# Kernel tuning notes

Measured on AMD Instinct MI355X. Metric: run time of the kernel, lower is better.

Reference implementation:

```python
import jax, jax.numpy as jnp
import numpy as np

N_NODES = 8      # objects per graph (fixed in source)
N_AT = 16        # anchors/targets vocab: 8 colors + 8 markers
H = 128          # n_hidden
BS = 16384


def _mlp(x, W1, b1, W2, b2):
    # layers.fully_connected default activation is relu; second layer linear.
    # dropout is identity in eval mode.
    return jax.nn.relu(x @ W1 + b1) @ W2 + b2


def _edges_and_segments(bs):
    # static edge list: all ordered pairs (i,j), i != j, per graph, offset per batch
    ii, jj = np.meshgrid(np.arange(N_NODES), np.arange(N_NODES), indexing='ij')
    m = ii != jj
    base = np.stack([ii[m], jj[m]], axis=1)                      # [56, 2]
    offs = (np.arange(bs) * N_NODES)[:, None, None]
    edges = (base[None] + offs).reshape(-1, 2).astype(np.int32)  # [bs*56, 2]
    seg_ids = np.repeat(np.arange(bs), N_NODES).astype(np.int32) # [bs*8]
    return jnp.asarray(edges), jnp.asarray(seg_ids)


def setup_inputs() -> dict:
    key = jax.random.key(0)
    ks = jax.random.split(key, 14)

    anchors = jax.random.randint(ks[0], (BS,), 0, N_AT)
    n_jumps = jax.random.randint(ks[1], (BS,), 0, N_NODES)
    positions = jax.random.uniform(ks[2], (BS, N_NODES, 2), dtype=jnp.float32)
    colors = jax.random.randint(ks[3], (BS, N_NODES), 0, 8)
    markers = jax.random.randint(ks[4], (BS, N_NODES), 8, 16)  # markers live in [8,16)

    def lin(k, fan_in, fan_out):
        return jax.random.normal(k, (fan_in, fan_out), dtype=jnp.float32) / np.sqrt(fan_in)

    d_in = 2 + 8 + 8 + N_AT + N_NODES  # pos + color_oh + marker_oh + question(16+8) = 42
    z = lambda n: jnp.zeros((n,), jnp.float32)
    return {
        'anchors': anchors, 'n_jumps': n_jumps, 'positions': positions,
        'colors': colors, 'markers': markers,
        'pre_W1': lin(ks[5], d_in, H),     'pre_b1': z(H),
        'pre_W2': lin(ks[6], H, H),        'pre_b2': z(H),
        'msg_W1': lin(ks[7], 2 * H + 1, H),'msg_b1': z(H),
        'msg_W2': lin(ks[8], H, H),        'msg_b2': z(H),
        'post_W1': lin(ks[9], 2 * H, H),   'post_b1': z(H),
        'post_W2': lin(ks[10], H, H),      'post_b2': z(H),
        'out_W1': lin(ks[11], H, H),       'out_b1': z(H),
        'out_W2': lin(ks[12], H, N_AT),    'out_b2': z(N_AT),
    }


def reference(anchors, n_jumps, positions, colors, markers,
              pre_W1, pre_b1, pre_W2, pre_b2,
              msg_W1, msg_b1, msg_W2, msg_b2,
              post_W1, post_b1, post_W2, post_b2,
              out_W1, out_b1, out_W2, out_b2):
    bs = positions.shape[0]
    edges, seg_ids = _edges_and_segments(bs)
    n_total = bs * N_NODES

    col_oh = jax.nn.one_hot(colors, 8, dtype=jnp.float32).reshape(n_total, 8)
    mrk_oh = jax.nn.one_hot(markers - 8, 8, dtype=jnp.float32).reshape(n_total, 8)
    pos = positions.reshape(n_total, 2)

    # pairwise euclidean distance per edge -> [E, 1]
    dp = pos[edges[:, 0]] - pos[edges[:, 1]]
    dist = jnp.sqrt(jnp.sum(dp * dp, axis=1, keepdims=True))

    # question broadcast to every node of its graph
    q = jnp.concatenate([jax.nn.one_hot(anchors, N_AT, dtype=jnp.float32),
                         jax.nn.one_hot(n_jumps, N_NODES, dtype=jnp.float32)], axis=1)
    q = q[seg_ids]  # [bs*8, 24]

    x0 = _mlp(jnp.concatenate([pos, col_oh, mrk_oh, q], axis=1),
              pre_W1, pre_b1, pre_W2, pre_b2)  # [bs*8, H]

    # one message-passing step: gather -> MLP -> scatter(segment_sum on source idx)
    mi = jnp.concatenate([x0[edges[:, 0]], x0[edges[:, 1]], dist], axis=1)  # [E, 257]
    msgs = _mlp(mi, msg_W1, msg_b1, msg_W2, msg_b2)                          # [E, H]
    upd = jax.ops.segment_sum(msgs, edges[:, 0], num_segments=n_total)       # [bs*8, H]

    x = _mlp(jnp.concatenate([upd, x0], axis=1), post_W1, post_b1, post_W2, post_b2)

    logits = jax.ops.segment_sum(x, seg_ids, num_segments=bs)  # [bs, H]
    logits = _mlp(logits, out_W1, out_b1, out_W2, out_b2)      # [bs, 16]
    return logits
```

## Files before the change

### kernel.cpp

```cpp
#include <hip/hip_runtime.h>

#define LROW 136
#define FSTR 72

typedef __bf16 bf16x8  __attribute__((ext_vector_type(8)));
typedef __bf16 bf16x2v __attribute__((ext_vector_type(2)));
typedef float  f32x4   __attribute__((ext_vector_type(4)));
typedef float  f32x2   __attribute__((ext_vector_type(2)));

#define MFMA16(a, b, c) __builtin_amdgcn_mfma_f32_16x16x32_bf16((a), (b), (c), 0, 0, 0)

__device__ __forceinline__ float bflo(unsigned v) { return __uint_as_float(v << 16); }
__device__ __forceinline__ float bfhi(unsigned v) { return __uint_as_float(v & 0xffff0000u); }

__device__ __forceinline__ unsigned short f2bf_u16(float f) {
  unsigned u = __float_as_uint(f);
  u += 0x7fffu + ((u >> 16) & 1u);
  return (unsigned short)(u >> 16);
}

__global__ void combine_weights(
    const float* __restrict__ pre_W1, const float* __restrict__ pre_b1,
    const float* __restrict__ pre_W2, const float* __restrict__ msg_W1,
    const float* __restrict__ msg_W2, const float* __restrict__ post_W1,
    const float* __restrict__ post_W2, const float* __restrict__ out_W1,
    const float* __restrict__ out_W2, const float* __restrict__ pre_b2,
    const float* __restrict__ msg_b1, const float* __restrict__ msg_b2,
    const float* __restrict__ post_b1, const float* __restrict__ post_b2,
    const float* __restrict__ out_b1,
    unsigned short* __restrict__ WabT, unsigned short* __restrict__ WdT,
    unsigned short* __restrict__ WcT, unsigned short* __restrict__ WoT,
    unsigned short* __restrict__ Wo2T, unsigned short* __restrict__ W1pT,
    float* __restrict__ vecs)
{
  __shared__ float part[256];
  const int b = blockIdx.x;
  const int t = threadIdx.x;
  if (b < 320) {
    const int p  = b >> 6;
    const int kp = b & 63;
    const int k  = kp * 2 + (t >> 7);
    const int n  = t & 127;
    const float* L; const float* R; unsigned short* O;
    if (p == 0)      { L = pre_W2;  R = msg_W1;             O = WabT; }
    else if (p == 1) { L = pre_W2;  R = msg_W1 + 128*128;   O = WabT + 128*128; }
    else if (p == 2) { L = pre_W2;  R = post_W1 + 128*128;  O = WdT; }
    else if (p == 3) { L = msg_W2;  R = post_W1;            O = WcT; }
    else             { L = post_W2; R = out_W1;             O = WoT; }
    const float* Lr = L + k * 128;
    float a0 = 0.f, a1 = 0.f, a2 = 0.f, a3 = 0.f;
    #pragma unroll 8
    for (int m = 0; m < 128; m += 4) {
      a0 = fmaf(Lr[m + 0], R[(m + 0) * 128 + n], a0);
      a1 = fmaf(Lr[m + 1], R[(m + 1) * 128 + n], a1);
      a2 = fmaf(Lr[m + 2], R[(m + 2) * 128 + n], a2);
      a3 = fmaf(Lr[m + 3], R[(m + 3) * 128 + n], a3);
    }
    O[n * 128 + k] = f2bf_u16((a0 + a1) + (a2 + a3));
  } else if (b == 320) {
    for (int idx = t; idx < 16 * 128; idx += 256) {
      int o = idx >> 7, k = idx & 127;
      Wo2T[o * 128 + k] = f2bf_u16(out_W2[k * 16 + o]);
    }
    if (t < 128) vecs[t] = msg_W1[256 * 128 + t];
    for (int idx = t; idx < 128 * 64; idx += 256) {
      int n = idx >> 6, k = idx & 63;
      float v = (k < 42) ? pre_W1[k * 128 + n] : (k == 42 ? pre_b1[n] : 0.f);
      W1pT[n * 64 + k] = f2bf_u16(v);
    }
  } else {
    const int n = t & 127;
    const int h = t >> 7;
    float s = 0.f;
    if (b == 321) {
      #pragma unroll 8
      for (int m = h * 64; m < h * 64 + 64; ++m)
        s = fmaf(pre_b2[m], msg_W1[m * 128 + n] + msg_W1[(128 + m) * 128 + n], s);
    } else if (b == 322) {
      #pragma unroll 8
      for (int m = h * 64; m < h * 64 + 64; ++m) {
        s = fmaf(7.f * msg_b2[m], post_W1[m * 128 + n], s);
        s = fmaf(pre_b2[m], post_W1[(128 + m) * 128 + n], s);
      }
    } else {
      #pragma unroll 8
      for (int m = h * 64; m < h * 64 + 64; ++m)
        s = fmaf(8.f * post_b2[m], out_W1[m * 128 + n], s);
    }
    part[t] = s;
    __syncthreads();
    if (t < 128) {
      float r = part[t] + part[t + 128];
      if (b == 321)      vecs[128 + t] = r + msg_b1[t];
      else if (b == 322) vecs[256 + t] = r + post_b1[t];
      else               vecs[384 + t] = r + out_b1[t];
    }
  }
}

__global__ void __launch_bounds__(256, 4) rrn_main(
    const int* __restrict__ anchors, const int* __restrict__ n_jumps,
    const float* __restrict__ positions, const int* __restrict__ colors,
    const int* __restrict__ markers,
    const __bf16* __restrict__ W1pT,
    const __bf16* __restrict__ WabT, const __bf16* __restrict__ WdT,
    const __bf16* __restrict__ WcT, const __bf16* __restrict__ WoT,
    const __bf16* __restrict__ Wo2T, const float* __restrict__ vecs,
    const float* __restrict__ out_b2, float* __restrict__ out)
{
  __shared__ __align__(16) char smem[38912];
  __bf16* featL = (__bf16*)(smem);
  __bf16* Ab    = (__bf16*)(smem);
  __bf16* h1    = (__bf16*)(smem + 17408);
  __bf16* Bb    = (__bf16*)(smem + 17408);
  __bf16* Sph   = (__bf16*)(smem + 17408);
  __bf16* hob   = (__bf16*)(smem + 21760);
  float*  dist  = (float*)(smem + 34816);
  float*  vec   = (float*)(smem + 36864);

  const int tid  = threadIdx.x;
  const int lane = tid & 63;
  const int w    = tid >> 6;
  const int l15  = lane & 15;
  const int quad = lane >> 4;
  const int colw = w * 32;
  const int g0   = blockIdx.x * 8;
  const int n0   = blockIdx.x * 64;

  if (tid < 64) {
    uint4* rp = (uint4*)&featL[tid * FSTR];
    uint4 z4 = {0u, 0u, 0u, 0u};
    #pragma unroll
    for (int i = 0; i < 9; ++i) rp[i] = z4;
    int g = tid >> 3;
    float px = positions[(n0 + tid) * 2], py = positions[(n0 + tid) * 2 + 1];
    int c  = colors[n0 + tid], mk = markers[n0 + tid] - 8;
    int a  = anchors[g0 + g],  nj = n_jumps[g0 + g];
    __bf16* row = &featL[tid * FSTR];
    row[0] = (__bf16)px; row[1] = (__bf16)py;
    const __bf16 one = (__bf16)1.f;
    row[2 + c] = one; row[10 + mk] = one;
    row[18 + a] = one; row[34 + nj] = one;
    row[42] = one;
  }
  for (int i = tid; i < 512; i += 256) {
    int g = i >> 6, ii = (i >> 3) & 7, jj = i & 7;
    const float* pa = positions + (n0 + g * 8 + ii) * 2;
    const float* pb = positions + (n0 + g * 8 + jj) * 2;
    float dx = pa[0] - pb[0], dy = pa[1] - pb[1];
    dist[i] = sqrtf(dx * dx + dy * dy);
  }
  for (int i = tid; i < 512; i += 256) vec[i] = vecs[i];
  __syncthreads();

  {
    f32x4 acch[4][2];
    f32x4 zero = {0.f, 0.f, 0.f, 0.f};
    #pragma unroll
    for (int mt = 0; mt < 4; ++mt) { acch[mt][0] = zero; acch[mt][1] = zero; }
    #pragma unroll
    for (int kb = 0; kb < 64; kb += 32) {
      const int ko = kb + quad * 8;
      bf16x8 fa[4], fb[2];
      #pragma unroll
      for (int mt = 0; mt < 4; ++mt)
        fa[mt] = *(const bf16x8*)&featL[(mt * 16 + l15) * FSTR + ko];
      fb[0] = *(const bf16x8*)&W1pT[(colw + l15) * 64 + ko];
      fb[1] = *(const bf16x8*)&W1pT[(colw + 16 + l15) * 64 + ko];
      #pragma unroll
      for (int mt = 0; mt < 4; ++mt) {
        acch[mt][0] = MFMA16(fa[mt], fb[0], acch[mt][0]);
        acch[mt][1] = MFMA16(fa[mt], fb[1], acch[mt][1]);
      }
    }
    __syncthreads();
    #pragma unroll
    for (int mt = 0; mt < 4; ++mt)
      #pragma unroll
      for (int nt = 0; nt < 2; ++nt) {
        int col = colw + nt * 16 + l15;
        #pragma unroll
        for (int r = 0; r < 4; ++r)
          h1[(mt * 16 + quad * 4 + r) * LROW + col] = (__bf16)fmaxf(acch[mt][nt][r], 0.f);
      }
  }
  __syncthreads();

  f32x4 acc1[4][4];
  {
    f32x4 zero = {0.f, 0.f, 0.f, 0.f};
    #pragma unroll
    for (int mt = 0; mt < 4; ++mt)
      #pragma unroll
      for (int nt = 0; nt < 4; ++nt) acc1[mt][nt] = zero;
  }
  #pragma unroll
  for (int kb = 0; kb < 128; kb += 32) {
    const int ko = kb + quad * 8;
    bf16x8 fa[4], fb[4];
    #pragma unroll
    for (int mt = 0; mt < 4; ++mt)
      fa[mt] = *(const bf16x8*)&h1[(mt * 16 + l15) * LROW + ko];
    fb[0] = *(const bf16x8*)&WabT[(colw + l15) * 128 + ko];
    fb[1] = *(const bf16x8*)&WabT[(colw + 16 + l15) * 128 + ko];
    fb[2] = *(const bf16x8*)&WabT[(128 + colw + l15) * 128 + ko];
    fb[3] = *(const bf16x8*)&WabT[(128 + colw + 16 + l15) * 128 + ko];
    #pragma unroll
    for (int mt = 0; mt < 4; ++mt)
      #pragma unroll
      for (int nt = 0; nt < 4; ++nt)
        acc1[mt][nt] = MFMA16(fa[mt], fb[nt], acc1[mt][nt]);
  }
  #pragma unroll
  for (int mt = 0; mt < 4; ++mt)
    #pragma unroll
    for (int nt = 0; nt < 2; ++nt) {
      int col = colw + nt * 16 + l15;
      #pragma unroll
      for (int r = 0; r < 4; ++r)
        Ab[(mt * 16 + quad * 4 + r) * LROW + col] = (__bf16)acc1[mt][nt][r];
    }

  f32x4 accD[4][2];
  {
    f32x4 zero = {0.f, 0.f, 0.f, 0.f};
    #pragma unroll
    for (int mt = 0; mt < 4; ++mt) { accD[mt][0] = zero; accD[mt][1] = zero; }
  }
  #pragma unroll
  for (int kb = 0; kb < 128; kb += 32) {
    const int ko = kb + quad * 8;
    bf16x8 fa[4], fd[2];
    #pragma unroll
    for (int mt = 0; mt < 4; ++mt)
      fa[mt] = *(const bf16x8*)&h1[(mt * 16 + l15) * LROW + ko];
    fd[0] = *(const bf16x8*)&WdT[(colw + l15) * 128 + ko];
    fd[1] = *(const bf16x8*)&WdT[(colw + 16 + l15) * 128 + ko];
    #pragma unroll
    for (int mt = 0; mt < 4; ++mt) {
      accD[mt][0] = MFMA16(fa[mt], fd[0], accD[mt][0]);
      accD[mt][1] = MFMA16(fa[mt], fd[1], accD[mt][1]);
    }
  }
  __syncthreads();
  #pragma unroll
  for (int mt = 0; mt < 4; ++mt)
    #pragma unroll
    for (int nt = 2; nt < 4; ++nt) {
      int col = colw + (nt - 2) * 16 + l15;
      #pragma unroll
      for (int r = 0; r < 4; ++r)
        Bb[(mt * 16 + quad * 4 + r) * LROW + col] = (__bf16)acc1[mt][nt][r];
    }
  __syncthreads();

  {
    const int g   = tid >> 5;
    const int nb4 = (tid & 31) * 4;
    const f32x2 w0 = *(const f32x2*)&vec[nb4];
    const f32x2 w1 = *(const f32x2*)&vec[nb4 + 2];
    const f32x2 c0 = *(const f32x2*)&vec[128 + nb4];
    const f32x2 c1 = *(const f32x2*)&vec[128 + nb4 + 2];
    const f32x2 z2 = {0.f, 0.f};
    f32x2 B0[8], B1[8];
    #pragma unroll
    for (int j = 0; j < 8; ++j) {
      uint2 vb = *(const uint2*)&Bb[(g * 8 + j) * LROW + nb4];
      B0[j].x = bflo(vb.x); B0[j].y = bfhi(vb.x);
      B1[j].x = bflo(vb.y); B1[j].y = bfhi(vb.y);
    }
    #pragma unroll
    for (int i = 0; i < 8; ++i) {
      uint2 va = *(const uint2*)&Ab[(g * 8 + i) * LROW + nb4];
      f32x2 a0; a0.x = bflo(va.x); a0.y = bfhi(va.x); a0 += c0;
      f32x2 a1; a1.x = bflo(va.y); a1.y = bfhi(va.y); a1 += c1;
      f32x2 s0 = z2, s1 = z2;
      #pragma unroll
      for (int j = 0; j < 8; ++j) {
        if (j == i) continue;
        float d = dist[g * 64 + i * 8 + j];
        f32x2 d2 = {d, d};
        f32x2 t0 = __builtin_elementwise_fma(d2, w0, B0[j]) + a0;
        f32x2 t1 = __builtin_elementwise_fma(d2, w1, B1[j]) + a1;
        t0 = __builtin_elementwise_max(t0, z2);
        t1 = __builtin_elementwise_max(t1, z2);
        s0 += t0; s1 += t1;
      }
      unsigned o0 = (unsigned)f2bf_u16(s0.x) | ((unsigned)f2bf_u16(s0.y) << 16);
      unsigned o1 = (unsigned)f2bf_u16(s1.x) | ((unsigned)f2bf_u16(s1.y) << 16);
      uint2 o = {o0, o1};
      *(uint2*)&Ab[(g * 8 + i) * LROW + nb4] = o;
    }
  }
  __syncthreads();

  {
    const __bf16* Sb = Ab;
    #pragma unroll
    for (int kb = 0; kb < 128; kb += 32) {
      const int ko = kb + quad * 8;
      bf16x8 fa[4], fc[2];
      #pragma unroll
      for (int mt = 0; mt < 4; ++mt)
        fa[mt] = *(const bf16x8*)&Sb[(mt * 16 + l15) * LROW + ko];
      fc[0] = *(const bf16x8*)&WcT[(colw + l15) * 128 + ko];
      fc[1] = *(const bf16x8*)&WcT[(colw + 16 + l15) * 128 + ko];
      #pragma unroll
      for (int mt = 0; mt < 4; ++mt) {
        accD[mt][0] = MFMA16(fa[mt], fc[0], accD[mt][0]);
        accD[mt][1] = MFMA16(fa[mt], fc[1], accD[mt][1]);
      }
    }
    #pragma unroll
    for (int mt = 0; mt < 4; ++mt)
      #pragma unroll
      for (int dt = 0; dt < 2; ++dt) {
        int col = colw + dt * 16 + l15;
        float cp = vec[256 + col];
        f32x4 a = accD[mt][dt];
        float s = fmaxf(a[0] + cp, 0.f) + fmaxf(a[1] + cp, 0.f)
                + fmaxf(a[2] + cp, 0.f) + fmaxf(a[3] + cp, 0.f);
        s += __shfl_xor(s, 16);
        int grow = mt * 2 + (lane >= 32 ? 1 : 0);
        if ((lane & 31) < 16) Sph[grow * LROW + col] = (__bf16)s;
        else                  Sph[(8 + grow) * LROW + col] = (__bf16)0.f;
      }
  }
  __syncthreads();

  {
    f32x4 acco[2];
    f32x4 zero = {0.f, 0.f, 0.f, 0.f};
    acco[0] = zero; acco[1] = zero;
    #pragma unroll
    for (int kb = 0; kb < 128; kb += 32) {
      const int ko = kb + quad * 8;
      bf16x8 fa = *(const bf16x8*)&Sph[l15 * LROW + ko];
      bf16x8 fb0 = *(const bf16x8*)&WoT[(colw + l15) * 128 + ko];
      bf16x8 fb1 = *(const bf16x8*)&WoT[(colw + 16 + l15) * 128 + ko];
      acco[0] = MFMA16(fa, fb0, acco[0]);
      acco[1] = MFMA16(fa, fb1, acco[1]);
    }
    #pragma unroll
    for (int dt = 0; dt < 2; ++dt) {
      int col = colw + dt * 16 + l15;
      float co = vec[384 + col];
      #pragma unroll
      for (int r = 0; r < 4; ++r)
        hob[(quad * 4 + r) * LROW + col] = (__bf16)fmaxf(acco[dt][r] + co, 0.f);
    }
  }
  __syncthreads();

  if (w == 0) {
    f32x4 accf = {0.f, 0.f, 0.f, 0.f};
    #pragma unroll
    for (int kb = 0; kb < 128; kb += 32) {
      const int ko = kb + quad * 8;
      bf16x8 fa  = *(const bf16x8*)&hob[l15 * LROW + ko];
      bf16x8 fbv = *(const bf16x8*)&Wo2T[l15 * 128 + ko];
      accf = MFMA16(fa, fbv, accf);
    }
    if (quad < 2) {
      float b2 = out_b2[l15];
      #pragma unroll
      for (int r = 0; r < 4; ++r) {
        int row = quad * 4 + r;
        out[(g0 + row) * 16 + l15] = accf[r] + b2;
      }
    }
  }
}

extern "C" void kernel_launch(void* const* d_in, const int* in_sizes, int n_in,
                              void* d_out, int out_size, void* d_ws, size_t ws_size,
                              hipStream_t stream) {
  const int*   anchors   = (const int*)d_in[0];
  const int*   n_jumps   = (const int*)d_in[1];
  const float* positions = (const float*)d_in[2];
  const int*   colors    = (const int*)d_in[3];
  const int*   markers   = (const int*)d_in[4];
  const float* pre_W1  = (const float*)d_in[5];
  const float* pre_b1  = (const float*)d_in[6];
  const float* pre_W2  = (const float*)d_in[7];
  const float* pre_b2  = (const float*)d_in[8];
  const float* msg_W1  = (const float*)d_in[9];
  const float* msg_b1  = (const float*)d_in[10];
  const float* msg_W2  = (const float*)d_in[11];
  const float* msg_b2  = (const float*)d_in[12];
  const float* post_W1 = (const float*)d_in[13];
  const float* post_b1 = (const float*)d_in[14];
  const float* post_W2 = (const float*)d_in[15];
  const float* post_b2 = (const float*)d_in[16];
  const float* out_W1  = (const float*)d_in[17];
  const float* out_b1  = (const float*)d_in[18];
  const float* out_W2  = (const float*)d_in[19];
  const float* out_b2  = (const float*)d_in[20];

  char* ws = (char*)d_ws;
  unsigned short* WabT = (unsigned short*)(ws);
  unsigned short* WdT  = (unsigned short*)(ws + 65536);
  unsigned short* WcT  = (unsigned short*)(ws + 98304);
  unsigned short* WoT  = (unsigned short*)(ws + 131072);
  unsigned short* Wo2T = (unsigned short*)(ws + 163840);
  float*          vecs = (float*)(ws + 167936);
  unsigned short* W1pT = (unsigned short*)(ws + 169984);

  const int BS = in_sizes[0];

  combine_weights<<<324, 256, 0, stream>>>(
      pre_W1, pre_b1, pre_W2, msg_W1, msg_W2, post_W1, post_W2, out_W1, out_W2,
      pre_b2, msg_b1, msg_b2, post_b1, post_b2, out_b1,
      WabT, WdT, WcT, WoT, Wo2T, W1pT, vecs);

  rrn_main<<<BS / 8, 256, 0, stream>>>(
      anchors, n_jumps, positions, colors, markers,
      (const __bf16*)W1pT,
      (const __bf16*)WabT, (const __bf16*)WdT, (const __bf16*)WcT,
      (const __bf16*)WoT, (const __bf16*)Wo2T, vecs, out_b2, (float*)d_out);
}
```

Baseline: 152.5 us.

## Split rrn_main work across 512 threads with row/column wave tiling

Doubles the block size from 256 to 512 threads. Each of the 8 waves now owns a 32-row by 32-column tile instead of all 64 rows by 32 columns. The pairwise message stage uses one graph per wave with 2 columns per lane, and the output layer uses 16 columns per wave. This cuts per-thread accumulator registers and raises the number of waves per CU to hide latency. In exchange, B-operand weight fragments are loaded twice as often across the block and barriers span more waves.

After: 183.8 us. 20.6% more time.

```diff
diff --git a/kernel.cpp b/kernel.cpp
--- a/kernel.cpp
+++ b/kernel.cpp
@@ -4,7 +4,6 @@
 #define FSTR 72
 
 typedef __bf16 bf16x8  __attribute__((ext_vector_type(8)));
-typedef __bf16 bf16x2v __attribute__((ext_vector_type(2)));
 typedef float  f32x4   __attribute__((ext_vector_type(4)));
 typedef float  f32x2   __attribute__((ext_vector_type(2)));
 
@@ -98,7 +97,7 @@
   }
 }
 
-__global__ void __launch_bounds__(256, 4) rrn_main(
+__global__ void __launch_bounds__(512, 6) rrn_main(
     const int* __restrict__ anchors, const int* __restrict__ n_jumps,
     const float* __restrict__ positions, const int* __restrict__ colors,
     const int* __restrict__ markers,
@@ -123,7 +122,9 @@
   const int w    = tid >> 6;
   const int l15  = lane & 15;
   const int quad = lane >> 4;
-  const int colw = w * 32;
+  const int rh   = w & 1;
+  const int rowh = rh * 32;
+  const int colq = (w >> 1) * 32;
   const int g0   = blockIdx.x * 8;
   const int n0   = blockIdx.x * 64;
 
@@ -143,153 +144,142 @@
     row[18 + a] = one; row[34 + nj] = one;
     row[42] = one;
   }
-  for (int i = tid; i < 512; i += 256) {
+  {
+    int i = tid;
     int g = i >> 6, ii = (i >> 3) & 7, jj = i & 7;
     const float* pa = positions + (n0 + g * 8 + ii) * 2;
     const float* pb = positions + (n0 + g * 8 + jj) * 2;
     float dx = pa[0] - pb[0], dy = pa[1] - pb[1];
     dist[i] = sqrtf(dx * dx + dy * dy);
   }
-  for (int i = tid; i < 512; i += 256) vec[i] = vecs[i];
-  __syncthreads();
-
-  {
-    f32x4 acch[4][2];
+  vec[tid] = vecs[tid];
+  __syncthreads();
+
+  {
+    f32x4 acch[2][2];
     f32x4 zero = {0.f, 0.f, 0.f, 0.f};
-    #pragma unroll
-    for (int mt = 0; mt < 4; ++mt) { acch[mt][0] = zero; acch[mt][1] = zero; }
+    acch[0][0] = zero; acch[0][1] = zero; acch[1][0] = zero; acch[1][1] = zero;
     #pragma unroll
     for (int kb = 0; kb < 64; kb += 32) {
       const int ko = kb + quad * 8;
-      bf16x8 fa[4], fb[2];
-      #pragma unroll
-      for (int mt = 0; mt < 4; ++mt)
-        fa[mt] = *(const bf16x8*)&featL[(mt * 16 + l15) * FSTR + ko];
-      fb[0] = *(const bf16x8*)&W1pT[(colw + l15) * 64 + ko];
-      fb[1] = *(const bf16x8*)&W1pT[(colw + 16 + l15) * 64 + ko];
-      #pragma unroll
-      for (int mt = 0; mt < 4; ++mt) {
+      bf16x8 fa[2], fb[2];
+      fa[0] = *(const bf16x8*)&featL[(rowh + l15) * FSTR + ko];
+      fa[1] = *(const bf16x8*)&featL[(rowh + 16 + l15) * FSTR + ko];
+      fb[0] = *(const bf16x8*)&W1pT[(colq + l15) * 64 + ko];
+      fb[1] = *(const bf16x8*)&W1pT[(colq + 16 + l15) * 64 + ko];
+      #pragma unroll
+      for (int mt = 0; mt < 2; ++mt) {
         acch[mt][0] = MFMA16(fa[mt], fb[0], acch[mt][0]);
         acch[mt][1] = MFMA16(fa[mt], fb[1], acch[mt][1]);
       }
     }
-    __syncthreads();
-    #pragma unroll
-    for (int mt = 0; mt < 4; ++mt)
+    #pragma unroll
+    for (int mt = 0; mt < 2; ++mt)
       #pragma unroll
       for (int nt = 0; nt < 2; ++nt) {
-        int col = colw + nt * 16 + l15;
+        int col = colq + nt * 16 + l15;
         #pragma unroll
         for (int r = 0; r < 4; ++r)
-          h1[(mt * 16 + quad * 4 + r) * LROW + col] = (__bf16)fmaxf(acch[mt][nt][r], 0.f);
-      }
-  }
-  __syncthreads();
-
-  f32x4 acc1[4][4];
+          h1[(rowh + mt * 16 + quad * 4 + r) * LROW + col] =
+              (__bf16)fmaxf(acch[mt][nt][r], 0.f);
+      }
+  }
+  __syncthreads();
+
+  f32x4 acc1[2][4];
   {
     f32x4 zero = {0.f, 0.f, 0.f, 0.f};
     #pragma unroll
-    for (int mt = 0; mt < 4; ++mt)
+    for (int mt = 0; mt < 2; ++mt)
       #pragma unroll
       for (int nt = 0; nt < 4; ++nt) acc1[mt][nt] = zero;
   }
   #pragma unroll
   for (int kb = 0; kb < 128; kb += 32) {
     const int ko = kb + quad * 8;
-    bf16x8 fa[4], fb[4];
-    #pragma unroll
-    for (int mt = 0; mt < 4; ++mt)
-      fa[mt] = *(const bf16x8*)&h1[(mt * 16 + l15) * LROW + ko];
-    fb[0] = *(const bf16x8*)&WabT[(colw + l15) * 128 + ko];
-    fb[1] = *(const bf16x8*)&WabT[(colw + 16 + l15) * 128 + ko];
-    fb[2] = *(const bf16x8*)&WabT[(128 + colw + l15) * 128 + ko];
-    fb[3] = *(const bf16x8*)&WabT[(128 + colw + 16 + l15) * 128 + ko];
-    #pragma unroll
-    for (int mt = 0; mt < 4; ++mt)
+    bf16x8 fa[2], fb[4];
+    fa[0] = *(const bf16x8*)&h1[(rowh + l15) * LROW + ko];
+    fa[1] = *(const bf16x8*)&h1[(rowh + 16 + l15) * LROW + ko];
+    fb[0] = *(const bf16x8*)&WabT[(colq + l15) * 128 + ko];
+    fb[1] = *(const bf16x8*)&WabT[(colq + 16 + l15) * 128 + ko];
+    fb[2] = *(const bf16x8*)&WabT[(128 + colq + l15) * 128 + ko];
+    fb[3] = *(const bf16x8*)&WabT[(128 + colq + 16 + l15) * 128 + ko];
+    #pragma unroll
+    for (int mt = 0; mt < 2; ++mt)
       #pragma unroll
       for (int nt = 0; nt < 4; ++nt)
         acc1[mt][nt] = MFMA16(fa[mt], fb[nt], acc1[mt][nt]);
   }
   #pragma unroll
-  for (int mt = 0; mt < 4; ++mt)
+  for (int mt = 0; mt < 2; ++mt)
     #pragma unroll
     for (int nt = 0; nt < 2; ++nt) {
-      int col = colw + nt * 16 + l15;
+      int col = colq + nt * 16 + l15;
       #pragma unroll
       for (int r = 0; r < 4; ++r)
-        Ab[(mt * 16 + quad * 4 + r) * LROW + col] = (__bf16)acc1[mt][nt][r];
-    }
-
-  f32x4 accD[4][2];
+        Ab[(rowh + mt * 16 + quad * 4 + r) * LROW + col] = (__bf16)acc1[mt][nt][r];
+    }
+
+  f32x4 accD[2][2];
   {
     f32x4 zero = {0.f, 0.f, 0.f, 0.f};
-    #pragma unroll
-    for (int mt = 0; mt < 4; ++mt) { accD[mt][0] = zero; accD[mt][1] = zero; }
+    accD[0][0] = zero; accD[0][1] = zero; accD[1][0] = zero; accD[1][1] = zero;
   }
   #pragma unroll
   for (int kb = 0; kb < 128; kb += 32) {
     const int ko = kb + quad * 8;
-    bf16x8 fa[4], fd[2];
-    #pragma unroll
-    for (int mt = 0; mt < 4; ++mt)
-      fa[mt] = *(const bf16x8*)&h1[(mt * 16 + l15) * LROW + ko];
-    fd[0] = *(const bf16x8*)&WdT[(colw + l15) * 128 + ko];
-    fd[1] = *(const bf16x8*)&WdT[(colw + 16 + l15) * 128 + ko];
-    #pragma unroll
-    for (int mt = 0; mt < 4; ++mt) {
+    bf16x8 fa[2], fd[2];
+    fa[0] = *(const bf16x8*)&h1[(rowh + l15) * LROW + ko];
+    fa[1] = *(const bf16x8*)&h1[(rowh + 16 + l15) * LROW + ko];
+    fd[0] = *(const bf16x8*)&WdT[(colq + l15) * 128 + ko];
+    fd[1] = *(const bf16x8*)&WdT[(colq + 16 + l15) * 128 + ko];
+    #pragma unroll
+    for (int mt = 0; mt < 2; ++mt) {
       accD[mt][0] = MFMA16(fa[mt], fd[0], accD[mt][0]);
       accD[mt][1] = MFMA16(fa[mt], fd[1], accD[mt][1]);
     }
   }
   __syncthreads();
   #pragma unroll
-  for (int mt = 0; mt < 4; ++mt)
+  for (int mt = 0; mt < 2; ++mt)
     #pragma unroll
     for (int nt = 2; nt < 4; ++nt) {
-      int col = colw + (nt - 2) * 16 + l15;
+      int col = colq + (nt - 2) * 16 + l15;
       #pragma unroll
       for (int r = 0; r < 4; ++r)
-        Bb[(mt * 16 + quad * 4 + r) * LROW + col] = (__bf16)acc1[mt][nt][r];
-    }
-  __syncthreads();
-
-  {
-    const int g   = tid >> 5;
-    const int nb4 = (tid & 31) * 4;
-    const f32x2 w0 = *(const f32x2*)&vec[nb4];
-    const f32x2 w1 = *(const f32x2*)&vec[nb4 + 2];
-    const f32x2 c0 = *(const f32x2*)&vec[128 + nb4];
-    const f32x2 c1 = *(const f32x2*)&vec[128 + nb4 + 2];
+        Bb[(rowh + mt * 16 + quad * 4 + r) * LROW + col] = (__bf16)acc1[mt][nt][r];
+    }
+  __syncthreads();
+
+  {
+    const int g   = w;
+    const int nb2 = lane * 2;
+    const f32x2 w0 = *(const f32x2*)&vec[nb2];
+    const f32x2 c0 = *(const f32x2*)&vec[128 + nb2];
     const f32x2 z2 = {0.f, 0.f};
-    f32x2 B0[8], B1[8];
+    f32x2 B0[8];
     #pragma unroll
     for (int j = 0; j < 8; ++j) {
-      uint2 vb = *(const uint2*)&Bb[(g * 8 + j) * LROW + nb4];
-      B0[j].x = bflo(vb.x); B0[j].y = bfhi(vb.x);
-      B1[j].x = bflo(vb.y); B1[j].y = bfhi(vb.y);
+      unsigned vb = *(const unsigned*)&Bb[(g * 8 + j) * LROW + nb2];
+      B0[j].x = bflo(vb); B0[j].y = bfhi(vb);
     }
     #pragma unroll
     for (int i = 0; i < 8; ++i) {
-      uint2 va = *(const uint2*)&Ab[(g * 8 + i) * LROW + nb4];
-      f32x2 a0; a0.x = bflo(va.x); a0.y = bfhi(va.x); a0 += c0;
-      f32x2 a1; a1.x = bflo(va.y); a1.y = bfhi(va.y); a1 += c1;
-      f32x2 s0 = z2, s1 = z2;
+      unsigned va = *(const unsigned*)&Ab[(g * 8 + i) * LROW + nb2];
+      f32x2 a0 = {bflo(va), bfhi(va)};
+      a0 += c0;
+      f32x2 s0 = z2;
       #pragma unroll
       for (int j = 0; j < 8; ++j) {
         if (j == i) continue;
         float d = dist[g * 64 + i * 8 + j];
         f32x2 d2 = {d, d};
         f32x2 t0 = __builtin_elementwise_fma(d2, w0, B0[j]) + a0;
-        f32x2 t1 = __builtin_elementwise_fma(d2, w1, B1[j]) + a1;
         t0 = __builtin_elementwise_max(t0, z2);
-        t1 = __builtin_elementwise_max(t1, z2);
-        s0 += t0; s1 += t1;
-      }
-      unsigned o0 = (unsigned)f2bf_u16(s0.x) | ((unsigned)f2bf_u16(s0.y) << 16);
-      unsigned o1 = (unsigned)f2bf_u16(s1.x) | ((unsigned)f2bf_u16(s1.y) << 16);
-      uint2 o = {o0, o1};
-      *(uint2*)&Ab[(g * 8 + i) * LROW + nb4] = o;
+        s0 += t0;
+      }
+      unsigned o = (unsigned)f2bf_u16(s0.x) | ((unsigned)f2bf_u16(s0.y) << 16);
+      *(unsigned*)&Ab[(g * 8 + i) * LROW + nb2] = o;
     }
   }
   __syncthreads();
@@ -299,56 +289,49 @@
     #pragma unroll
     for (int kb = 0; kb < 128; kb += 32) {
       const int ko = kb + quad * 8;
-      bf16x8 fa[4], fc[2];
-      #pragma unroll
-      for (int mt = 0; mt < 4; ++mt)
-        fa[mt] = *(const bf16x8*)&Sb[(mt * 16 + l15) * LROW + ko];
-      fc[0] = *(const bf16x8*)&WcT[(colw + l15) * 128 + ko];
-      fc[1] = *(const bf16x8*)&WcT[(colw + 16 + l15) * 128 + ko];
-      #pragma unroll
-      for (int mt = 0; mt < 4; ++mt) {
+      bf16x8 fa[2], fc[2];
+      fa[0] = *(const bf16x8*)&Sb[(rowh + l15) * LROW + ko];
+      fa[1] = *(const bf16x8*)&Sb[(rowh + 16 + l15) * LROW + ko];
+      fc[0] = *(const bf16x8*)&WcT[(colq + l15) * 128 + ko];
+      fc[1] = *(const bf16x8*)&WcT[(colq + 16 + l15) * 128 + ko];
+      #pragma unroll
+      for (int mt = 0; mt < 2; ++mt) {
         accD[mt][0] = MFMA16(fa[mt], fc[0], accD[mt][0]);
         accD[mt][1] = MFMA16(fa[mt], fc[1], accD[mt][1]);
       }
     }
     #pragma unroll
-    for (int mt = 0; mt < 4; ++mt)
+    for (int mt = 0; mt < 2; ++mt)
       #pragma unroll
       for (int dt = 0; dt < 2; ++dt) {
-        int col = colw + dt * 16 + l15;
+        int col = colq + dt * 16 + l15;
         float cp = vec[256 + col];
         f32x4 a = accD[mt][dt];
         float s = fmaxf(a[0] + cp, 0.f) + fmaxf(a[1] + cp, 0.f)
                 + fmaxf(a[2] + cp, 0.f) + fmaxf(a[3] + cp, 0.f);
         s += __shfl_xor(s, 16);
-        int grow = mt * 2 + (lane >= 32 ? 1 : 0);
-        if ((lane & 31) < 16) Sph[grow * LROW + col] = (__bf16)s;
-        else                  Sph[(8 + grow) * LROW + col] = (__bf16)0.f;
-      }
-  }
-  __syncthreads();
-
-  {
-    f32x4 acco[2];
-    f32x4 zero = {0.f, 0.f, 0.f, 0.f};
-    acco[0] = zero; acco[1] = zero;
+        int graph = rh * 4 + mt * 2 + (lane >= 32 ? 1 : 0);
+        if ((lane & 31) < 16) Sph[graph * LROW + col] = (__bf16)s;
+        else                  Sph[(8 + graph) * LROW + col] = (__bf16)0.f;
+      }
+  }
+  __syncthreads();
+
+  {
+    const int colw6 = w * 16;
+    f32x4 acco = {0.f, 0.f, 0.f, 0.f};
     #pragma unroll
     for (int kb = 0; kb < 128; kb += 32) {
       const int ko = kb + quad * 8;
-      bf16x8 fa = *(const bf16x8*)&Sph[l15 * LROW + ko];
-      bf16x8 fb0 = *(const bf16x8*)&WoT[(colw + l15) * 128 + ko];
-      bf16x8 fb1 = *(const bf16x8*)&WoT[(colw + 16 + l15) * 128 + ko];
-      acco[0] = MFMA16(fa, fb0, acco[0]);
-      acco[1] = MFMA16(fa, fb1, acco[1]);
-    }
-    #pragma unroll
-    for (int dt = 0; dt < 2; ++dt) {
-      int col = colw + dt * 16 + l15;
-      float co = vec[384 + col];
-      #pragma unroll
-      for (int r = 0; r < 4; ++r)
-        hob[(quad * 4 + r) * LROW + col] = (__bf16)fmaxf(acco[dt][r] + co, 0.f);
-    }
+      bf16x8 fa  = *(const bf16x8*)&Sph[l15 * LROW + ko];
+      bf16x8 fbv = *(const bf16x8*)&WoT[(colw6 + l15) * 128 + ko];
+      acco = MFMA16(fa, fbv, acco);
+    }
+    int col = colw6 + l15;
+    float co = vec[384 + col];
+    #pragma unroll
+    for (int r = 0; r < 4; ++r)
+      hob[(quad * 4 + r) * LROW + col] = (__bf16)fmaxf(acco[r] + co, 0.f);
   }
   __syncthreads();
 
@@ -413,7 +396,7 @@
       pre_b2, msg_b1, msg_b2, post_b1, post_b2, out_b1,
       WabT, WdT, WcT, WoT, Wo2T, W1pT, vecs);
 
-  rrn_main<<<BS / 8, 256, 0, stream>>>(
+  rrn_main<<<BS / 8, 512, 0, stream>>>(
       anchors, n_jumps, positions, colors, markers,
       (const __bf16*)W1pT,
       (const __bf16*)WabT, (const __bf16*)WdT, (const __bf16*)WcT,
```

## Remap pairwise message stage to MFMA-owned columns and drop barriers

Applied to the files above, without the earlier changes.

The pairwise relu-sum stage now has each thread process the same columns and row group it wrote from its own MFMA accumulators, instead of a different row/column assignment. That lets the barrier between writing Bb and reading it be removed, and a redundant barrier before the h1 store is also dropped. Each thread now handles two graphs with 2 columns each instead of one graph with 4 columns. The risks are correctness if any thread reads Ab/Bb entries written by other lanes without a barrier, and narrower 4-byte LDS accesses.

Result: no change. 154.6 us, median of 2 (+1.4%).

```diff
diff --git a/kernel.cpp b/kernel.cpp
--- a/kernel.cpp
+++ b/kernel.cpp
@@ -4,7 +4,6 @@
 #define FSTR 72
 
 typedef __bf16 bf16x8  __attribute__((ext_vector_type(8)));
-typedef __bf16 bf16x2v __attribute__((ext_vector_type(2)));
 typedef float  f32x4   __attribute__((ext_vector_type(4)));
 typedef float  f32x2   __attribute__((ext_vector_type(2)));
 
@@ -173,7 +172,6 @@
         acch[mt][1] = MFMA16(fa[mt], fb[1], acch[mt][1]);
       }
     }
-    __syncthreads();
     #pragma unroll
     for (int mt = 0; mt < 4; ++mt)
       #pragma unroll
@@ -181,7 +179,8 @@
         int col = colw + nt * 16 + l15;
         #pragma unroll
         for (int r = 0; r < 4; ++r)
-          h1[(mt * 16 + quad * 4 + r) * LROW + col] = (__bf16)fmaxf(acch[mt][nt][r], 0.f);
+          h1[(mt * 16 + quad * 4 + r) * LROW + col] =
+              (__bf16)fmaxf(acch[mt][nt][r], 0.f);
       }
   }
   __syncthreads();
@@ -252,44 +251,37 @@
       for (int r = 0; r < 4; ++r)
         Bb[(mt * 16 + quad * 4 + r) * LROW + col] = (__bf16)acc1[mt][nt][r];
     }
-  __syncthreads();
-
-  {
-    const int g   = tid >> 5;
-    const int nb4 = (tid & 31) * 4;
-    const f32x2 w0 = *(const f32x2*)&vec[nb4];
-    const f32x2 w1 = *(const f32x2*)&vec[nb4 + 2];
-    const f32x2 c0 = *(const f32x2*)&vec[128 + nb4];
-    const f32x2 c1 = *(const f32x2*)&vec[128 + nb4 + 2];
+
+  {
+    const int c0 = colw + ((l15 & 8) << 1) + 2 * (l15 & 7);
+    const f32x2 wv = { vec[c0], vec[c0 + 1] };
+    const f32x2 cv = { vec[128 + c0], vec[128 + c0 + 1] };
     const f32x2 z2 = {0.f, 0.f};
-    f32x2 B0[8], B1[8];
-    #pragma unroll
-    for (int j = 0; j < 8; ++j) {
-      uint2 vb = *(const uint2*)&Bb[(g * 8 + j) * LROW + nb4];
-      B0[j].x = bflo(vb.x); B0[j].y = bfhi(vb.x);
-      B1[j].x = bflo(vb.y); B1[j].y = bfhi(vb.y);
-    }
-    #pragma unroll
-    for (int i = 0; i < 8; ++i) {
-      uint2 va = *(const uint2*)&Ab[(g * 8 + i) * LROW + nb4];
-      f32x2 a0; a0.x = bflo(va.x); a0.y = bfhi(va.x); a0 += c0;
-      f32x2 a1; a1.x = bflo(va.y); a1.y = bfhi(va.y); a1 += c1;
-      f32x2 s0 = z2, s1 = z2;
+    #pragma unroll
+    for (int gi = 0; gi < 2; ++gi) {
+      const int g = 2 * quad + gi;
+      f32x2 Bj[8];
       #pragma unroll
       for (int j = 0; j < 8; ++j) {
-        if (j == i) continue;
-        float d = dist[g * 64 + i * 8 + j];
-        f32x2 d2 = {d, d};
-        f32x2 t0 = __builtin_elementwise_fma(d2, w0, B0[j]) + a0;
-        f32x2 t1 = __builtin_elementwise_fma(d2, w1, B1[j]) + a1;
-        t0 = __builtin_elementwise_max(t0, z2);
-        t1 = __builtin_elementwise_max(t1, z2);
-        s0 += t0; s1 += t1;
-      }
-      unsigned o0 = (unsigned)f2bf_u16(s0.x) | ((unsigned)f2bf_u16(s0.y) << 16);
-      unsigned o1 = (unsigned)f2bf_u16(s1.x) | ((unsigned)f2bf_u16(s1.y) << 16);
-      uint2 o = {o0, o1};
-      *(uint2*)&Ab[(g * 8 + i) * LROW + nb4] = o;
+        unsigned vb = *(const unsigned*)&Bb[(g * 8 + j) * LROW + c0];
+        Bj[j].x = bflo(vb); Bj[j].y = bfhi(vb);
+      }
+      #pragma unroll
+      for (int i = 0; i < 8; ++i) {
+        unsigned va = *(const unsigned*)&Ab[(g * 8 + i) * LROW + c0];
+        f32x2 a = {bflo(va) + cv.x, bfhi(va) + cv.y};
+        f32x2 s = z2;
+        #pragma unroll
+        for (int j = 0; j < 8; ++j) {
+          if (j == i) continue;
+          float d = dist[g * 64 + i * 8 + j];
+          f32x2 d2 = {d, d};
+          f32x2 t = __builtin_elementwise_fma(d2, wv, Bj[j]) + a;
+          s += __builtin_elementwise_max(t, z2);
+        }
+        unsigned o = (unsigned)f2bf_u16(s.x) | ((unsigned)f2bf_u16(s.y) << 16);
+        *(unsigned*)&Ab[(g * 8 + i) * LROW + c0] = o;
+      }
     }
   }
   __syncthreads();
```
